# Performance work log

Hardware: AMD Instinct MI355X
Metric: run time of the kernel (lower is better)

Reference implementation:

```python
import jax, jax.numpy as jnp
import numpy as np

BLKQ = 64
BLKK = 64
TOPK_RATIO = 0.2


def setup_inputs() -> dict:
    key = jax.random.key(0)
    ks = jax.random.split(key, 5)
    B, H, L, D = 1, 16, 2048, 64
    q = jax.random.normal(ks[0], (B, H, L, D), dtype=jnp.float32)
    k = jax.random.normal(ks[1], (B, H, L, D), dtype=jnp.float32)
    v = jax.random.normal(ks[2], (B, H, L, D), dtype=jnp.float32)
    # proj_l params (zero-init in source; random here so the branch is exercised)
    W_proj = jax.random.normal(ks[3], (D, D), dtype=jnp.float32) * 0.02
    b_proj = jax.random.normal(ks[4], (D,), dtype=jnp.float32) * 0.02
    return {"q": q, "k": k, "v": v, "W_proj": W_proj, "b_proj": b_proj}


def _block_lut(q, k, topk_ratio, blkq, blkk):
    # q,k: [B,H,L,D]. Mean-pool blocks, score, take top-k key blocks per query block.
    B, H, L, D = q.shape
    M, N = L // blkq, L // blkk
    q_blocks = q.reshape(B, H, M, blkq, D).mean(axis=3)   # [B,H,M,D]
    k_blocks = k.reshape(B, H, N, blkk, D).mean(axis=3)   # [B,H,N,D]
    block_scores = jnp.einsum("bhmd,bhnd->bhmn", q_blocks, k_blocks)
    topk = min(N, max(1, int(topk_ratio * N)))
    _, lut = jax.lax.top_k(block_scores, topk)            # [B,H,M,topk] int32
    return lut, topk, M, N


def reference(q, k, v, W_proj, b_proj):
    B, H, L, D = q.shape
    lut, topk, M, N = _block_lut(q, k, TOPK_RATIO, BLKQ, BLKK)

    # ---- block-sparse softmax attention ----
    block_mask = jnp.any(jax.nn.one_hot(lut, N, dtype=jnp.bool_), axis=3)  # [B,H,M,N]
    mask = jnp.repeat(jnp.repeat(block_mask, BLKQ, axis=2), BLKK, axis=3)  # [B,H,L,L]
    scale = 1.0 / jnp.sqrt(jnp.asarray(D, q.dtype))
    scores = jnp.einsum("bhld,bhkd->bhlk", q, k) * scale
    scores = jnp.where(mask, scores, -jnp.inf)
    attn = jax.nn.softmax(scores, axis=-1)  # every row has >= topk*BLKK valid keys
    o_s = jnp.einsum("bhlk,bhkd->bhld", attn, v)

    # ---- linear attention (softmax feature map over D) ----
    q_feat = jax.nn.softmax(q, axis=-1)
    k_feat = jax.nn.softmax(k, axis=-1)
    kv_sum = jnp.einsum("bhld,bhle->bhde", k_feat, v)      # [B,H,D,D]
    k_sum = k_feat.sum(axis=2)                              # [B,H,D]
    num = jnp.einsum("bhld,bhde->bhle", q_feat, kv_sum)
    den = jnp.einsum("bhld,bhd->bhl", q_feat, k_sum)[..., None] + 1e-5
    o_l = num / den
    o_l = jnp.einsum("bhld,ed->bhle", o_l, W_proj) + b_proj  # nn.Linear: x @ W.T + b

    return o_s + o_l
```

## Files before the change

kernel.cpp:

```cpp
#include <hip/hip_runtime.h>
#include <math.h>

#define Hh 16
#define Ll 2048
#define Dd 64
#define MB 32
#define TK 6

typedef __attribute__((ext_vector_type(8))) short s16x8;
typedef __attribute__((ext_vector_type(4))) short s16x4;
typedef __attribute__((ext_vector_type(4))) float f32x4;

static __device__ __forceinline__ unsigned short f2bf(float x) {
  unsigned int u = __float_as_uint(x);
  return (unsigned short)((u + 0x7fffu + ((u >> 16) & 1u)) >> 16);
}
static __device__ __forceinline__ float bf2f(short b) {
  return __uint_as_float(((unsigned int)(unsigned short)b) << 16);
}
static __device__ __forceinline__ int swz(int row, int bcol) {
  return row * 128 + (bcol ^ ((row & 7) << 4));
}

__global__ __launch_bounds__(256)
void k_prep(const float* __restrict__ q, const float* __restrict__ k,
            const float* __restrict__ v,
            unsigned short* __restrict__ qbf, unsigned short* __restrict__ kbf,
            unsigned short* __restrict__ vt,
            float* __restrict__ qb, float* __restrict__ kb,
            unsigned short* __restrict__ part_kv, float* __restrict__ part_ks) {
  __shared__ float tile[64][65];
  __shared__ float kf_s[64][68];
  __shared__ float v_sh[64][68];
  int hm = blockIdx.x;
  int h = hm >> 5;
  int t = threadIdx.x;
  int r = t >> 2, c0 = (t & 3) * 16;
  const size_t base = (size_t)hm * (64 * Dd);
  int m = hm & 31;

  {
    float4 f[4];
#pragma unroll
    for (int i = 0; i < 4; ++i) {
      f[i] = *(const float4*)(q + base + r * Dd + c0 + i * 4);
      *(float4*)&tile[r][c0 + i * 4] = f[i];
      float4 vv = *(const float4*)(v + base + r * Dd + c0 + i * 4);
      *(float4*)&v_sh[r][c0 + i * 4] = vv;
    }
    const float* ff = (const float*)f;
    unsigned short* dst = qbf + base;
#pragma unroll
    for (int halfi = 0; halfi < 2; ++halfi) {
      s16x8 o;
#pragma unroll
      for (int j = 0; j < 8; ++j) o[j] = (short)f2bf(ff[halfi * 8 + j] * 0.125f);
      *(s16x8*)(dst + r * Dd + c0 + halfi * 8) = o;
    }
  }
  __syncthreads();
  if (t < 64) {
    float s = 0.f;
#pragma unroll 8
    for (int rr = 0; rr < 64; ++rr) s += tile[rr][t];
    qb[hm * 64 + t] = s * (1.0f / 64.0f);
  }
  {
    int d = t >> 2, kc = (t & 3) * 16;
    unsigned short* dst = vt + (size_t)h * Dd * Ll + (size_t)d * Ll + m * 64 + kc;
#pragma unroll
    for (int halfi = 0; halfi < 2; ++halfi) {
      s16x8 o;
#pragma unroll
      for (int j = 0; j < 8; ++j) o[j] = (short)f2bf(v_sh[kc + halfi * 8 + j][d]);
      *(s16x8*)(dst + halfi * 8) = o;
    }
  }
  __syncthreads();

  {
    float4 f[4];
#pragma unroll
    for (int i = 0; i < 4; ++i) {
      f[i] = *(const float4*)(k + base + r * Dd + c0 + i * 4);
      *(float4*)&tile[r][c0 + i * 4] = f[i];
    }
    const float* ff = (const float*)f;
    unsigned short* dst = kbf + base;
#pragma unroll
    for (int halfi = 0; halfi < 2; ++halfi) {
      s16x8 o;
#pragma unroll
      for (int j = 0; j < 8; ++j) o[j] = (short)f2bf(ff[halfi * 8 + j]);
      *(s16x8*)(dst + r * Dd + c0 + halfi * 8) = o;
    }
  }
  __syncthreads();
  if (t < 64) {
    float s = 0.f;
#pragma unroll 8
    for (int rr = 0; rr < 64; ++rr) s += tile[rr][t];
    kb[hm * 64 + t] = s * (1.0f / 64.0f);
  }
  {
    int rg = t >> 4;
    int c4 = (t & 15) * 4;
#pragma unroll
    for (int ch = 0; ch < 4; ++ch) {
      int rl = ch * 16 + rg;
      float4 kq = *(const float4*)&tile[rl][c4];
      float mx = fmaxf(fmaxf(kq.x, kq.y), fmaxf(kq.z, kq.w));
#pragma unroll
      for (int off = 8; off; off >>= 1) mx = fmaxf(mx, __shfl_xor(mx, off));
      float ex = __expf(kq.x - mx), ey = __expf(kq.y - mx);
      float ez = __expf(kq.z - mx), ew = __expf(kq.w - mx);
      float sm = ex + ey + ez + ew;
#pragma unroll
      for (int off = 8; off; off >>= 1) sm += __shfl_xor(sm, off);
      float inv = 1.0f / sm;
      *(float4*)&kf_s[rl][c4] = make_float4(ex * inv, ey * inv, ez * inv, ew * inv);
    }
  }
  __syncthreads();
  {
    int da0 = (t >> 4) * 4, e0 = (t & 15) * 4;
    float kvacc[4][4] = {};
    float ks4[4] = {0.f, 0.f, 0.f, 0.f};
    for (int rr = 0; rr < 64; ++rr) {
      float4 kf = *(const float4*)&kf_s[rr][da0];
      float4 vv = *(const float4*)&v_sh[rr][e0];
      ks4[0] += kf.x; ks4[1] += kf.y; ks4[2] += kf.z; ks4[3] += kf.w;
      kvacc[0][0] += kf.x * vv.x; kvacc[0][1] += kf.x * vv.y; kvacc[0][2] += kf.x * vv.z; kvacc[0][3] += kf.x * vv.w;
      kvacc[1][0] += kf.y * vv.x; kvacc[1][1] += kf.y * vv.y; kvacc[1][2] += kf.y * vv.z; kvacc[1][3] += kf.y * vv.w;
      kvacc[2][0] += kf.z * vv.x; kvacc[2][1] += kf.z * vv.y; kvacc[2][2] += kf.z * vv.z; kvacc[2][3] += kf.z * vv.w;
      kvacc[3][0] += kf.w * vv.x; kvacc[3][1] += kf.w * vv.y; kvacc[3][2] += kf.w * vv.z; kvacc[3][3] += kf.w * vv.w;
    }
    unsigned short* pkv = part_kv + (size_t)hm * 4096;
#pragma unroll
    for (int i = 0; i < 4; ++i) {
      s16x4 o;
      o[0] = (short)f2bf(kvacc[i][0]); o[1] = (short)f2bf(kvacc[i][1]);
      o[2] = (short)f2bf(kvacc[i][2]); o[3] = (short)f2bf(kvacc[i][3]);
      *(s16x4*)(pkv + (da0 + i) * 64 + e0) = o;
    }
    if ((t & 15) == 0) {
#pragma unroll
      for (int i = 0; i < 4; ++i) part_ks[hm * 64 + da0 + i] = ks4[i];
    }
  }
}

__global__ __launch_bounds__(256)
void k_topk_fold(const float* __restrict__ qb, const float* __restrict__ kb,
                 int* __restrict__ lut,
                 const unsigned short* __restrict__ part_kv, const float* __restrict__ part_ks,
                 const float* __restrict__ W, float* __restrict__ ksum,
                 unsigned short* __restrict__ kvwt) {
  __shared__ float kvr[16][68];
  __shared__ float w_s[64][65];
  int blk = blockIdx.x;
  int t = threadIdx.x;
  if (blk < 128) {
    int w = t >> 6, l = t & 63;
    int hm = blk * 4 + w;
    int hh = hm >> 5;
    float val = -INFINITY;
    if (l < 32) {
      const float* qv = qb + hm * 64;
      const float* kv = kb + (hh * 32 + l) * 64;
      float s = 0.f;
#pragma unroll
      for (int d4 = 0; d4 < 16; ++d4) {
        float4 a = *(const float4*)(qv + d4 * 4);
        float4 bb = *(const float4*)(kv + d4 * 4);
        s += a.x * bb.x + a.y * bb.y + a.z * bb.z + a.w * bb.w;
      }
      val = s;
    }
    int idx = l & 31;
    for (int t6 = 0; t6 < TK; ++t6) {
      float bv = val; int bi = idx;
#pragma unroll
      for (int off = 32; off; off >>= 1) {
        float ov = __shfl_xor(bv, off);
        int oi = __shfl_xor(bi, off);
        if (ov > bv || (ov == bv && oi < bi)) { bv = ov; bi = oi; }
      }
      if (l == 0) lut[hm * TK + t6] = bi;
      if (idx == bi && l < 32) val = -INFINITY;
    }
  } else {
    int fidx = blk - 128;
    int h = fidx >> 2, qtr = fidx & 3;
    int a0 = qtr * 16;
    {
      int a = t >> 4, b4 = (t & 15) * 4;
      float4 acc = make_float4(0.f, 0.f, 0.f, 0.f);
      for (int cc = 0; cc < 32; ++cc) {
        s16x4 p = *(const s16x4*)(part_kv + (size_t)(h * 32 + cc) * 4096 + (a0 + a) * 64 + b4);
        acc.x += bf2f(p[0]); acc.y += bf2f(p[1]);
        acc.z += bf2f(p[2]); acc.w += bf2f(p[3]);
      }
      *(float4*)&kvr[a][b4] = acc;
      int r = t >> 2, cq = (t & 3) * 16;
#pragma unroll
      for (int j = 0; j < 16; ++j) w_s[r][cq + j] = W[r * 64 + cq + j];
      if (qtr == 0 && t < 64) {
        float s = 0.f;
        for (int cc = 0; cc < 32; ++cc) s += part_ks[(h * 32 + cc) * 64 + t];
        ksum[h * 64 + t] = s;
      }
    }
    __syncthreads();
    int e = t & 63, ag = t >> 6;
    float acc4[4] = {0.f, 0.f, 0.f, 0.f};
    for (int b = 0; b < 64; ++b) {
      float wv = w_s[e][b];
#pragma unroll
      for (int i = 0; i < 4; ++i) acc4[i] += kvr[ag * 4 + i][b] * wv;
    }
#pragma unroll
    for (int i = 0; i < 4; ++i)
      kvwt[h * 4096 + e * 64 + a0 + ag * 4 + i] = f2bf(acc4[i]);
  }
}

__global__ __launch_bounds__(256, 2)
void k_attn(const unsigned short* __restrict__ qbf,
            const unsigned short* __restrict__ kbf,
            const unsigned short* __restrict__ vt,
            const int* __restrict__ lut,
            const unsigned short* __restrict__ kvwt,
            const float* __restrict__ ksum, const float* __restrict__ bproj,
            float* __restrict__ out) {
  __shared__ unsigned short k_s[2][4096];
  __shared__ unsigned short v_s[2][4096];
  __shared__ unsigned short p_s[4][1024];
  __shared__ unsigned short kvwt_s[4096];
  __shared__ float ks_s[64], b_s[64];
  __shared__ float den_s[4][16];

  int bid = blockIdx.x;
  int hm = (bid & 7) * 64 + (bid >> 3);
  int h = hm >> 5, m = hm & 31;
  int t = threadIdx.x, w = t >> 6, l = t & 63;
  int g = l >> 4, c16 = l & 15;

  int nbs[TK];
#pragma unroll
  for (int i = 0; i < TK; ++i) nbs[i] = lut[hm * TK + i];

  const unsigned short* kh = kbf + (size_t)h * Ll * Dd;
  const unsigned short* vh = vt + (size_t)h * Dd * Ll;

  auto stage = [&](int buf, int nb) {
    const unsigned short* kb = kh + nb * 64 * Dd;
    const unsigned short* vb = vh + nb * 64;
#pragma unroll
    for (int i = 0; i < 2; ++i) {
      int c = i * 256 + t;
      int row = c >> 3, sub = c & 7;
      int scol = (sub ^ (row & 7)) * 8;
      __builtin_amdgcn_global_load_lds(
          (const __attribute__((address_space(1))) void*)(kb + row * Dd + scol),
          (__attribute__((address_space(3))) void*)&k_s[buf][c * 8], 16, 0, 0);
    }
#pragma unroll
    for (int i = 0; i < 2; ++i) {
      int c = i * 256 + t;
      int row = c >> 3, sub = c & 7;
      int scol = (sub ^ (row & 7)) * 8;
      __builtin_amdgcn_global_load_lds(
          (const __attribute__((address_space(1))) void*)(vb + (size_t)row * Ll + scol),
          (__attribute__((address_space(3))) void*)&v_s[buf][c * 8], 16, 0, 0);
    }
  };

  stage(0, nbs[0]);

  const unsigned short* qg = qbf + ((size_t)h * Ll + m * 64) * Dd;
  s16x8 aq[2];
#pragma unroll
  for (int kc = 0; kc < 2; ++kc)
    aq[kc] = *(const s16x8*)(qg + (w * 16 + c16) * Dd + kc * 32 + g * 8);

#pragma unroll
  for (int cc = 0; cc < 2; ++cc) {
    int idx = t + cc * 256;
    int row = idx >> 3, col8 = idx & 7;
    s16x8 val = *(const s16x8*)(kvwt + h * 4096 + row * 64 + col8 * 8);
    *(s16x8*)&kvwt_s[swz(row, col8 * 16) >> 1] = val;
  }
  if (t < 64) { ks_s[t] = ksum[h * 64 + t]; b_s[t] = bproj[t]; }

  float mrow[4] = {-INFINITY, -INFINITY, -INFINITY, -INFINITY};
  float lrow[4] = {0.f, 0.f, 0.f, 0.f};
  f32x4 o[4] = {};

  for (int kbi = 0; kbi < TK; ++kbi) {
    int buf = kbi & 1;
    asm volatile("s_waitcnt vmcnt(0)" ::: "memory");
    __builtin_amdgcn_sched_barrier(0);
    __builtin_amdgcn_s_barrier();
    __builtin_amdgcn_sched_barrier(0);
    if (kbi + 1 < TK) stage(buf ^ 1, nbs[kbi + 1]);

    f32x4 s[4];
    __builtin_amdgcn_s_setprio(1);
#pragma unroll
    for (int nt = 0; nt < 4; ++nt) {
      s16x8 b0 = *(const s16x8*)&k_s[buf][swz(nt * 16 + c16, g * 16) >> 1];
      s16x8 b1 = *(const s16x8*)&k_s[buf][swz(nt * 16 + c16, 64 + g * 16) >> 1];
      f32x4 z = {0.f, 0.f, 0.f, 0.f};
      z = __builtin_amdgcn_mfma_f32_16x16x32_bf16(aq[0], b0, z, 0, 0, 0);
      s[nt] = __builtin_amdgcn_mfma_f32_16x16x32_bf16(aq[1], b1, z, 0, 0, 0);
    }
    __builtin_amdgcn_s_setprio(0);

#pragma unroll
    for (int r = 0; r < 4; ++r) {
      float mx = fmaxf(fmaxf(s[0][r], s[1][r]), fmaxf(s[2][r], s[3][r]));
#pragma unroll
      for (int off = 8; off; off >>= 1) mx = fmaxf(mx, __shfl_xor(mx, off));
      float nm = fmaxf(mrow[r], mx);
      float rs = __expf(mrow[r] - nm);
      float sum = 0.f;
      int qrow = g * 4 + r;
#pragma unroll
      for (int nt = 0; nt < 4; ++nt) {
        float pv = __expf(s[nt][r] - nm);
        sum += pv;
        p_s[w][swz(qrow, (nt * 16 + c16) * 2) >> 1] = f2bf(pv);
      }
#pragma unroll
      for (int off = 8; off; off >>= 1) sum += __shfl_xor(sum, off);
      lrow[r] = lrow[r] * rs + sum;
      mrow[r] = nm;
      o[0][r] *= rs; o[1][r] *= rs; o[2][r] *= rs; o[3][r] *= rs;
    }

    asm volatile("s_waitcnt lgkmcnt(0)" ::: "memory");
    __builtin_amdgcn_sched_barrier(0);

    s16x8 ap0 = *(const s16x8*)&p_s[w][swz(c16, g * 16) >> 1];
    s16x8 ap1 = *(const s16x8*)&p_s[w][swz(c16, 64 + g * 16) >> 1];
    __builtin_amdgcn_s_setprio(1);
#pragma unroll
    for (int nt = 0; nt < 4; ++nt) {
      s16x8 b0 = *(const s16x8*)&v_s[buf][swz(nt * 16 + c16, g * 16) >> 1];
      s16x8 b1 = *(const s16x8*)&v_s[buf][swz(nt * 16 + c16, 64 + g * 16) >> 1];
      o[nt] = __builtin_amdgcn_mfma_f32_16x16x32_bf16(ap0, b0, o[nt], 0, 0, 0);
      o[nt] = __builtin_amdgcn_mfma_f32_16x16x32_bf16(ap1, b1, o[nt], 0, 0, 0);
    }
    __builtin_amdgcn_s_setprio(0);
  }

  float qf0[8], qf1[8];
  float mx = -INFINITY;
#pragma unroll
  for (int j = 0; j < 8; ++j) {
    qf0[j] = bf2f(aq[0][j]) * 8.f;
    qf1[j] = bf2f(aq[1][j]) * 8.f;
    mx = fmaxf(mx, fmaxf(qf0[j], qf1[j]));
  }
  mx = fmaxf(mx, __shfl_xor(mx, 16));
  mx = fmaxf(mx, __shfl_xor(mx, 32));
  float sm = 0.f;
#pragma unroll
  for (int j = 0; j < 8; ++j) {
    qf0[j] = __expf(qf0[j] - mx);
    qf1[j] = __expf(qf1[j] - mx);
    sm += qf0[j] + qf1[j];
  }
  sm += __shfl_xor(sm, 16);
  sm += __shfl_xor(sm, 32);
  float qinv = 1.0f / sm;
  float dp = 0.f;
#pragma unroll
  for (int j = 0; j < 8; ++j) {
    qf0[j] *= qinv; qf1[j] *= qinv;
    dp += qf0[j] * ks_s[g * 8 + j] + qf1[j] * ks_s[32 + g * 8 + j];
  }
  dp += __shfl_xor(dp, 16);
  dp += __shfl_xor(dp, 32);
  if (g == 0) den_s[w][c16] = dp + 1e-5f;
  s16x8 pa0, pa1;
#pragma unroll
  for (int j = 0; j < 8; ++j) {
    pa0[j] = (short)f2bf(qf0[j]);
    pa1[j] = (short)f2bf(qf1[j]);
  }
  asm volatile("s_waitcnt lgkmcnt(0)" ::: "memory");
  __builtin_amdgcn_sched_barrier(0);

  f32x4 ol[4];
  __builtin_amdgcn_s_setprio(1);
#pragma unroll
  for (int nt = 0; nt < 4; ++nt) {
    s16x8 b0 = *(const s16x8*)&kvwt_s[swz(nt * 16 + c16, g * 16) >> 1];
    s16x8 b1 = *(const s16x8*)&kvwt_s[swz(nt * 16 + c16, 64 + g * 16) >> 1];
    f32x4 z = {0.f, 0.f, 0.f, 0.f};
    z = __builtin_amdgcn_mfma_f32_16x16x32_bf16(pa0, b0, z, 0, 0, 0);
    ol[nt] = __builtin_amdgcn_mfma_f32_16x16x32_bf16(pa1, b1, z, 0, 0, 0);
  }
  __builtin_amdgcn_s_setprio(0);

  float* ob = out + ((size_t)h * Ll + m * 64 + w * 16) * Dd;
#pragma unroll
  for (int r = 0; r < 4; ++r) {
    float inv_l = 1.0f / lrow[r];
    int qrow = g * 4 + r;
    float invd = 1.0f / den_s[w][qrow];
#pragma unroll
    for (int nt = 0; nt < 4; ++nt)
      ob[qrow * Dd + nt * 16 + c16] =
          o[nt][r] * inv_l + ol[nt][r] * invd + b_s[nt * 16 + c16];
  }
}

extern "C" void kernel_launch(void* const* d_in, const int* in_sizes, int n_in,
                              void* d_out, int out_size, void* d_ws, size_t ws_size,
                              hipStream_t stream) {
  const float* q = (const float*)d_in[0];
  const float* k = (const float*)d_in[1];
  const float* v = (const float*)d_in[2];
  const float* W = (const float*)d_in[3];
  const float* b = (const float*)d_in[4];
  float* out = (float*)d_out;

  char* wsb = (char*)d_ws;
  unsigned short* qbf = (unsigned short*)(wsb);
  unsigned short* kbf = (unsigned short*)(wsb + 4194304);
  unsigned short* vt  = (unsigned short*)(wsb + 8388608);
  float* qb      = (float*)(wsb + 12582912);
  float* kb      = (float*)(wsb + 12713984);
  int*   lut     = (int*)(wsb + 12845056);
  unsigned short* part_kv = (unsigned short*)(wsb + 12857344);
  float* part_ks = (float*)(wsb + 17051648);
  float* ksum    = (float*)(wsb + 17182720);
  unsigned short* kvwt = (unsigned short*)(wsb + 17186816);

  k_prep<<<512, 256, 0, stream>>>(q, k, v, qbf, kbf, vt, qb, kb,
                                  part_kv, part_ks);
  k_topk_fold<<<192, 256, 0, stream>>>(qb, kb, lut, part_kv, part_ks, W, ksum, kvwt);
  k_attn<<<512, 256, 0, stream>>>(qbf, kbf, vt, lut, kvwt, ksum, b, out);
}
```

Before: 42.03 us.

## Compute linear-attention KV state with MFMA in fold kernel instead of per-block partials

The prep kernel no longer computes per-block 64x64 K_feat^T V partial products with scalar FMAs. Instead it writes a transposed bf16 copy of the softmaxed K features. The fold kernel then computes the full per-head KV matrix with bf16 MFMA over all 2048 rows, reduces across four waves in shared memory, and applies the W projection with MFMA too. This drops scalar FMA work from prep and the partial-sum round trip. In exchange the fold phase runs only 16 head blocks doing long serial loops, which may leave the GPU underused, and it adds more bf16 rounding.

```diff
diff --git a/kernel.cpp b/kernel.cpp
--- a/kernel.cpp
+++ b/kernel.cpp
@@ -28,7 +28,7 @@
             unsigned short* __restrict__ qbf, unsigned short* __restrict__ kbf,
             unsigned short* __restrict__ vt,
             float* __restrict__ qb, float* __restrict__ kb,
-            unsigned short* __restrict__ part_kv, float* __restrict__ part_ks) {
+            unsigned short* __restrict__ kft, float* __restrict__ part_ks) {
   __shared__ float tile[64][65];
   __shared__ float kf_s[64][68];
   __shared__ float v_sh[64][68];
@@ -123,41 +123,35 @@
   }
   __syncthreads();
   {
-    int da0 = (t >> 4) * 4, e0 = (t & 15) * 4;
-    float kvacc[4][4] = {};
-    float ks4[4] = {0.f, 0.f, 0.f, 0.f};
-    for (int rr = 0; rr < 64; ++rr) {
-      float4 kf = *(const float4*)&kf_s[rr][da0];
-      float4 vv = *(const float4*)&v_sh[rr][e0];
-      ks4[0] += kf.x; ks4[1] += kf.y; ks4[2] += kf.z; ks4[3] += kf.w;
-      kvacc[0][0] += kf.x * vv.x; kvacc[0][1] += kf.x * vv.y; kvacc[0][2] += kf.x * vv.z; kvacc[0][3] += kf.x * vv.w;
-      kvacc[1][0] += kf.y * vv.x; kvacc[1][1] += kf.y * vv.y; kvacc[1][2] += kf.y * vv.z; kvacc[1][3] += kf.y * vv.w;
-      kvacc[2][0] += kf.z * vv.x; kvacc[2][1] += kf.z * vv.y; kvacc[2][2] += kf.z * vv.z; kvacc[2][3] += kf.z * vv.w;
-      kvacc[3][0] += kf.w * vv.x; kvacc[3][1] += kf.w * vv.y; kvacc[3][2] += kf.w * vv.z; kvacc[3][3] += kf.w * vv.w;
-    }
-    unsigned short* pkv = part_kv + (size_t)hm * 4096;
-#pragma unroll
-    for (int i = 0; i < 4; ++i) {
-      s16x4 o;
-      o[0] = (short)f2bf(kvacc[i][0]); o[1] = (short)f2bf(kvacc[i][1]);
-      o[2] = (short)f2bf(kvacc[i][2]); o[3] = (short)f2bf(kvacc[i][3]);
-      *(s16x4*)(pkv + (da0 + i) * 64 + e0) = o;
-    }
-    if ((t & 15) == 0) {
-#pragma unroll
-      for (int i = 0; i < 4; ++i) part_ks[hm * 64 + da0 + i] = ks4[i];
-    }
+    int d = t >> 2, kc = (t & 3) * 16;
+    unsigned short* dst = kft + (size_t)h * Dd * Ll + (size_t)d * Ll + m * 64 + kc;
+    float ssum = 0.f;
+#pragma unroll
+    for (int halfi = 0; halfi < 2; ++halfi) {
+      s16x8 o;
+#pragma unroll
+      for (int j = 0; j < 8; ++j) {
+        float val = kf_s[kc + halfi * 8 + j][d];
+        ssum += val;
+        o[j] = (short)f2bf(val);
+      }
+      *(s16x8*)(dst + halfi * 8) = o;
+    }
+    ssum += __shfl_xor(ssum, 1);
+    ssum += __shfl_xor(ssum, 2);
+    if ((t & 3) == 0) part_ks[hm * 64 + d] = ssum;
   }
 }
 
 __global__ __launch_bounds__(256)
 void k_topk_fold(const float* __restrict__ qb, const float* __restrict__ kb,
                  int* __restrict__ lut,
-                 const unsigned short* __restrict__ part_kv, const float* __restrict__ part_ks,
+                 const unsigned short* __restrict__ kft, const unsigned short* __restrict__ vt,
+                 const float* __restrict__ part_ks,
                  const float* __restrict__ W, float* __restrict__ ksum,
                  unsigned short* __restrict__ kvwt) {
-  __shared__ float kvr[16][68];
-  __shared__ float w_s[64][65];
+  __shared__ float red[4][64][68];
+  __shared__ unsigned short kvbf_s[4096];
   int blk = blockIdx.x;
   int t = threadIdx.x;
   if (blk < 128) {
@@ -190,38 +184,86 @@
       if (idx == bi && l < 32) val = -INFINITY;
     }
   } else {
-    int fidx = blk - 128;
-    int h = fidx >> 2, qtr = fidx & 3;
-    int a0 = qtr * 16;
+    int h = blk - 128;
+    int w = t >> 6, l = t & 63;
+    int g = l >> 4, c16 = l & 15;
+    const unsigned short* kfh = kft + (size_t)h * Dd * Ll;
+    const unsigned short* vth = vt + (size_t)h * Dd * Ll;
+
+    f32x4 acc[4][4] = {};
+    for (int cc = 0; cc < 16; ++cc) {
+      int l0 = (w * 16 + cc) * 32 + g * 8;
+      s16x8 af[4], bf[4];
+#pragma unroll
+      for (int dt = 0; dt < 4; ++dt)
+        af[dt] = *(const s16x8*)(kfh + (size_t)(dt * 16 + c16) * Ll + l0);
+#pragma unroll
+      for (int et = 0; et < 4; ++et)
+        bf[et] = *(const s16x8*)(vth + (size_t)(et * 16 + c16) * Ll + l0);
+#pragma unroll
+      for (int dt = 0; dt < 4; ++dt)
+#pragma unroll
+        for (int et = 0; et < 4; ++et)
+          acc[dt][et] = __builtin_amdgcn_mfma_f32_16x16x32_bf16(af[dt], bf[et], acc[dt][et], 0, 0, 0);
+    }
+#pragma unroll
+    for (int dt = 0; dt < 4; ++dt)
+#pragma unroll
+      for (int et = 0; et < 4; ++et)
+#pragma unroll
+        for (int r = 0; r < 4; ++r)
+          red[w][dt * 16 + g * 4 + r][et * 16 + c16] = acc[dt][et][r];
+    __syncthreads();
+
     {
-      int a = t >> 4, b4 = (t & 15) * 4;
-      float4 acc = make_float4(0.f, 0.f, 0.f, 0.f);
-      for (int cc = 0; cc < 32; ++cc) {
-        s16x4 p = *(const s16x4*)(part_kv + (size_t)(h * 32 + cc) * 4096 + (a0 + a) * 64 + b4);
-        acc.x += bf2f(p[0]); acc.y += bf2f(p[1]);
-        acc.z += bf2f(p[2]); acc.w += bf2f(p[3]);
-      }
-      *(float4*)&kvr[a][b4] = acc;
-      int r = t >> 2, cq = (t & 3) * 16;
-#pragma unroll
-      for (int j = 0; j < 16; ++j) w_s[r][cq + j] = W[r * 64 + cq + j];
-      if (qtr == 0 && t < 64) {
+      int a = t >> 2, eq = (t & 3) * 16;
+#pragma unroll
+      for (int halfi = 0; halfi < 2; ++halfi) {
+        s16x8 o;
+#pragma unroll
+        for (int j = 0; j < 8; ++j) {
+          int b = eq + halfi * 8 + j;
+          float s = red[0][a][b] + red[1][a][b] + red[2][a][b] + red[3][a][b];
+          o[j] = (short)f2bf(s);
+        }
+        *(s16x8*)&kvbf_s[swz(a, eq * 2 + halfi * 16) >> 1] = o;
+      }
+      if (t < 64) {
         float s = 0.f;
-        for (int cc = 0; cc < 32; ++cc) s += part_ks[(h * 32 + cc) * 64 + t];
+        for (int m = 0; m < 32; ++m) s += part_ks[(h * 32 + m) * 64 + t];
         ksum[h * 64 + t] = s;
       }
     }
     __syncthreads();
-    int e = t & 63, ag = t >> 6;
-    float acc4[4] = {0.f, 0.f, 0.f, 0.f};
-    for (int b = 0; b < 64; ++b) {
-      float wv = w_s[e][b];
-#pragma unroll
-      for (int i = 0; i < 4; ++i) acc4[i] += kvr[ag * 4 + i][b] * wv;
-    }
-#pragma unroll
-    for (int i = 0; i < 4; ++i)
-      kvwt[h * 4096 + e * 64 + a0 + ag * 4 + i] = f2bf(acc4[i]);
+
+    {
+      s16x8 aw[2];
+#pragma unroll
+      for (int kc = 0; kc < 2; ++kc) {
+        const float* p0 = W + (w * 16 + c16) * 64 + kc * 32 + g * 8;
+        float4 x = *(const float4*)p0, y = *(const float4*)(p0 + 4);
+        s16x8 a;
+        a[0] = (short)f2bf(x.x); a[1] = (short)f2bf(x.y);
+        a[2] = (short)f2bf(x.z); a[3] = (short)f2bf(x.w);
+        a[4] = (short)f2bf(y.x); a[5] = (short)f2bf(y.y);
+        a[6] = (short)f2bf(y.z); a[7] = (short)f2bf(y.w);
+        aw[kc] = a;
+      }
+      f32x4 ol[4];
+#pragma unroll
+      for (int at = 0; at < 4; ++at) {
+        s16x8 b0 = *(const s16x8*)&kvbf_s[swz(at * 16 + c16, g * 16) >> 1];
+        s16x8 b1 = *(const s16x8*)&kvbf_s[swz(at * 16 + c16, 64 + g * 16) >> 1];
+        f32x4 z = {0.f, 0.f, 0.f, 0.f};
+        z = __builtin_amdgcn_mfma_f32_16x16x32_bf16(aw[0], b0, z, 0, 0, 0);
+        ol[at] = __builtin_amdgcn_mfma_f32_16x16x32_bf16(aw[1], b1, z, 0, 0, 0);
+      }
+#pragma unroll
+      for (int at = 0; at < 4; ++at)
+#pragma unroll
+        for (int r = 0; r < 4; ++r)
+          kvwt[h * 4096 + (w * 16 + g * 4 + r) * 64 + at * 16 + c16] = f2bf(ol[at][r]);
+    }
   }
 }
 
@@ -435,13 +477,12 @@
   float* qb      = (float*)(wsb + 12582912);
   float* kb      = (float*)(wsb + 12713984);
   int*   lut     = (int*)(wsb + 12845056);
-  unsigned short* part_kv = (unsigned short*)(wsb + 12857344);
+  unsigned short* kft = (unsigned short*)(wsb + 12857344);
   float* part_ks = (float*)(wsb + 17051648);
   float* ksum    = (float*)(wsb + 17182720);
   unsigned short* kvwt = (unsigned short*)(wsb + 17186816);
 
-  k_prep<<<512, 256, 0, stream>>>(q, k, v, qbf, kbf, vt, qb, kb,
-                                  part_kv, part_ks);
-  k_topk_fold<<<192, 256, 0, stream>>>(qb, kb, lut, part_kv, part_ks, W, ksum, kvwt);
+  k_prep<<<512, 256, 0, stream>>>(q, k, v, qbf, kbf, vt, qb, kb, kft, part_ks);
+  k_topk_fold<<<144, 256, 0, stream>>>(qb, kb, lut, kft, vt, part_ks, W, ksum, kvwt);
   k_attn<<<512, 256, 0, stream>>>(qbf, kbf, vt, lut, kvwt, ksum, b, out);
 }
```

Result: slower. 51.51 us (+22.6%).
